# Optimization experiments

Measured on AMD Instinct MI355X. Metric: run time of the kernel, lower is better.

The kernel has to match this reference:

```python
import jax, jax.numpy as jnp
import numpy as np

D_MODEL = 1024
NUM_HEADS = 16
DEPTH = D_MODEL // NUM_HEADS


def setup_inputs() -> dict:
    key = jax.random.key(0)
    ks = jax.random.split(key, 9)
    B, S = 2, 2048
    s = 1.0 / np.sqrt(D_MODEL)
    return {
        "x": jax.random.normal(ks[0], (B, S, D_MODEL), dtype=jnp.float32),
        "wq": jax.random.normal(ks[1], (D_MODEL, D_MODEL), dtype=jnp.float32) * s,
        "bq": jnp.zeros((D_MODEL,), dtype=jnp.float32),
        "wk": jax.random.normal(ks[2], (D_MODEL, D_MODEL), dtype=jnp.float32) * s,
        "bk": jnp.zeros((D_MODEL,), dtype=jnp.float32),
        "wv": jax.random.normal(ks[3], (D_MODEL, D_MODEL), dtype=jnp.float32) * s,
        "bv": jnp.zeros((D_MODEL,), dtype=jnp.float32),
        "wo": jax.random.normal(ks[4], (D_MODEL, D_MODEL), dtype=jnp.float32) * s,
        "bo": jnp.zeros((D_MODEL,), dtype=jnp.float32),
    }


def _split_heads(t):
    # [B, S, D] -> [B, H, S, depth]
    B, S, _ = t.shape
    return t.reshape(B, S, NUM_HEADS, DEPTH).transpose(0, 2, 1, 3)


def reference(x, wq, bq, wk, bk, wv, bv, wo, bo):
    B, S, _ = x.shape
    q = _split_heads(x @ wq + bq)
    k = _split_heads(x @ wk + bk)
    v = _split_heads(x @ wv + bv)
    scale = 1.0 / jnp.sqrt(jnp.asarray(DEPTH, dtype=x.dtype))
    logits = jnp.einsum("bhsd,bhtd->bhst", q, k) * scale  # [B,H,S,S]
    attn = jax.nn.softmax(logits, axis=-1)
    ctx = jnp.einsum("bhst,bhtd->bhsd", attn, v)  # [B,H,S,depth]
    concat = ctx.transpose(0, 2, 1, 3).reshape(B, S, D_MODEL)
    return concat @ wo + bo
```

## Files before the change

### kernel.cpp

```cpp
#include <hip/hip_runtime.h>
#include <hip/hip_bf16.h>

typedef __bf16 bf16;
typedef __bf16 bf16x4 __attribute__((ext_vector_type(4)));
typedef __bf16 bf16x8 __attribute__((ext_vector_type(8)));
typedef float f32x4 __attribute__((ext_vector_type(4)));

typedef __attribute__((address_space(3))) void lds_void;
typedef const __attribute__((address_space(1))) void gbl_void;

#define D_MODEL 1024
#define NHEAD 16
#define DEPTH 64
#define SEQ 2048
#define BATCH 2
#define NTOK (BATCH * SEQ)

#define Q_SCALE 0.18033688f

__global__ __launch_bounds__(256) void prep(const float* __restrict__ w0,
                                            const float* __restrict__ w1,
                                            const float* __restrict__ w2,
                                            const float* __restrict__ w3,
                                            const float* __restrict__ x,
                                            bf16* __restrict__ wtb,
                                            bf16* __restrict__ xb) {
    int z = blockIdx.z;
    int tx = threadIdx.x, ty = threadIdx.y;
    if (z < 4) {
        const float* w = (z == 0) ? w0 : (z == 1) ? w1 : (z == 2) ? w2 : w3;
        bf16* d = wtb + (size_t)z * D_MODEL * D_MODEL;
        __shared__ float tile[32][33];
        int c0 = blockIdx.x * 32;
        int r0 = blockIdx.y * 32;
#pragma unroll
        for (int i = 0; i < 4; i++)
            tile[ty + i * 8][tx] = w[(size_t)(r0 + ty + i * 8) * D_MODEL + c0 + tx];
        __syncthreads();
#pragma unroll
        for (int i = 0; i < 4; i++)
            d[(size_t)(c0 + ty + i * 8) * D_MODEL + r0 + tx] = (bf16)tile[tx][ty + i * 8];
    } else {
        int t = ty * 32 + tx;
        size_t i = ((size_t)(z - 4) * 1024 + blockIdx.y * 32 + blockIdx.x) * 256 + t;
        float4 v = ((const float4*)x)[i];
        bf16x4 o = {(bf16)v.x, (bf16)v.y, (bf16)v.z, (bf16)v.w};
        *(bf16x4*)&xb[i * 4] = o;
    }
}

template <bool SWAP>
__device__ __forceinline__ void gemm_core128(const bf16* __restrict__ A,
                                             const bf16* __restrict__ Bt,
                                             int row0, int col0,
                                             bf16 (*sm)[2][8192],
                                             f32x4 acc[4][4]) {
    const int tid = threadIdx.x;
    const int lane = tid & 63;
    const int wave = tid >> 6;
    const int quad = lane >> 4, l16 = lane & 15;
    const int wm = (wave & 1) << 6, wn = (wave >> 1) << 6;
    const int sA = l16 & 7;
    const int scg = (tid & 7) ^ ((tid >> 3) & 7);

    const bf16* Ag = A + (size_t)(row0 + (tid >> 3)) * D_MODEL + scg * 8;
    const bf16* Bg = Bt + (size_t)(col0 + (tid >> 3)) * D_MODEL + scg * 8;

#define GLLQ(SRC, DST) __builtin_amdgcn_global_load_lds((gbl_void*)(SRC), (lds_void*)(DST), 16, 0, 0)
#define STGQ(BUF_, KB_) { \
    _Pragma("unroll") \
    for (int o_ = 0; o_ < 4; o_++) \
        GLLQ(Ag + (size_t)o_ * 32 * D_MODEL + (KB_), &sm[BUF_][0][o_ * 2048 + tid * 8]); \
    _Pragma("unroll") \
    for (int o_ = 0; o_ < 4; o_++) \
        GLLQ(Bg + (size_t)o_ * 32 * D_MODEL + (KB_), &sm[BUF_][1][o_ * 2048 + tid * 8]); }

    STGQ(0, 0);
#pragma unroll 1
    for (int t = 0; t < 16; t++) {
        if (t < 15) {
            STGQ((t + 1) & 1, (t + 1) * 64);
            asm volatile("s_waitcnt vmcnt(8)" ::: "memory");
        } else {
            asm volatile("s_waitcnt vmcnt(0)" ::: "memory");
        }
        __builtin_amdgcn_sched_barrier(0);
        __builtin_amdgcn_s_barrier();
        const int bs = t & 1;
#pragma unroll
        for (int kq = 0; kq < 2; kq++) {
            bf16x8 af[4], bfr[4];
            const int c = ((((kq << 2) | quad) ^ sA) << 3);
#pragma unroll
            for (int i = 0; i < 4; i++)
                af[i] = *(const bf16x8*)&sm[bs][0][(wm + i * 16 + l16) * 64 + c];
#pragma unroll
            for (int j = 0; j < 4; j++)
                bfr[j] = *(const bf16x8*)&sm[bs][1][(wn + j * 16 + l16) * 64 + c];
            __builtin_amdgcn_s_setprio(1);
#pragma unroll
            for (int i = 0; i < 4; i++)
#pragma unroll
                for (int j = 0; j < 4; j++)
                    acc[i][j] = SWAP
                        ? __builtin_amdgcn_mfma_f32_16x16x32_bf16(bfr[j], af[i], acc[i][j], 0, 0, 0)
                        : __builtin_amdgcn_mfma_f32_16x16x32_bf16(af[i], bfr[j], acc[i][j], 0, 0, 0);
            __builtin_amdgcn_s_setprio(0);
        }
        __builtin_amdgcn_sched_barrier(0);
        __builtin_amdgcn_s_barrier();
    }
#undef STGQ
#undef GLLQ
}

__global__ __launch_bounds__(256) void qkv_gemm(const bf16* __restrict__ xb,
                                                const bf16* __restrict__ wtb,
                                                const float* __restrict__ bq,
                                                const float* __restrict__ bk,
                                                const float* __restrict__ bv,
                                                bf16* __restrict__ q,
                                                bf16* __restrict__ k,
                                                bf16* __restrict__ v) {
    __shared__ __align__(16) bf16 sm[2][2][8192];
    int zc = blockIdx.x;
    int z = zc >> 3;
    const bf16* Bt = wtb + (size_t)z * D_MODEL * D_MODEL;
    const float* bias = (z == 0) ? bq : (z == 1) ? bk : bv;
    int row0 = blockIdx.y * 128, col0 = (zc & 7) * 128;
    f32x4 acc[4][4] = {};

    const int lane = threadIdx.x & 63, wave = threadIdx.x >> 6;
    const int quad = lane >> 4, l16 = lane & 15;
    const int wm = (wave & 1) << 6, wn = (wave >> 1) << 6;

    if (z < 2) {
        gemm_core128<false>(xb, Bt, row0, col0, sm, acc);
        bf16* dst = (z == 0) ? q : k;
        const float sc = (z == 0) ? Q_SCALE : 1.0f;
#pragma unroll
        for (int i = 0; i < 4; i++) {
#pragma unroll
            for (int j = 0; j < 4; j++) {
                int colg = col0 + wn + j * 16 + l16;
                int hh = colg >> 6, d = colg & 63;
                float bi = bias[colg];
                int rbase = row0 + wm + i * 16 + quad * 4;
                int b = rbase >> 11, sb = rbase & 2047;
#pragma unroll
                for (int r = 0; r < 4; r++) {
                    size_t idx = ((size_t)(b * NHEAD + hh) * SEQ + sb + r) * DEPTH + d;
                    dst[idx] = (bf16)((acc[i][j][r] + bi) * sc);
                }
            }
        }
    } else {
        gemm_core128<true>(xb, Bt, row0, col0, sm, acc);
#pragma unroll
        for (int i = 0; i < 4; i++) {
            int tok = row0 + wm + i * 16 + l16;
            int b = tok >> 11, sb = tok & 2047;
#pragma unroll
            for (int j = 0; j < 4; j++) {
#pragma unroll
                for (int r = 0; r < 4; r++) {
                    int f = col0 + wn + j * 16 + quad * 4 + r;
                    int hh = f >> 6, d = f & 63;
                    v[((size_t)(b * NHEAD + hh) * DEPTH + d) * SEQ + sb] =
                        (bf16)(acc[i][j][r] + bias[f]);
                }
            }
        }
    }
}

__global__ __launch_bounds__(512, 4) void attn(const bf16* __restrict__ q,
                                               const bf16* __restrict__ k,
                                               const bf16* __restrict__ v,
                                               bf16* __restrict__ ctx) {
    __shared__ __align__(16) bf16 smb[32768];
    const int tid = threadIdx.x;
    const int lane = tid & 63, wave = tid >> 6;
    const int ks = wave & 3, qg = wave >> 2;
    const int quad = lane >> 4, l16 = lane & 15;
    const int bh = blockIdx.x;
    const int q0 = blockIdx.y * 64;
    const size_t hb = (size_t)bh * SEQ * DEPTH;
    const bf16* qh = q + hb;
    const bf16* kh = k + hb;
    const bf16* vh = v + hb;

    bf16x8 bq_[2][2];
#pragma unroll
    for (int n = 0; n < 2; n++) {
        int qrow = q0 + qg * 32 + n * 16 + l16;
#pragma unroll
        for (int c = 0; c < 2; c++)
            bq_[n][c] = *(const bf16x8*)&qh[(size_t)qrow * DEPTH + c * 32 + quad * 8];
    }

    f32x4 ov[4][2] = {};
    float lvs[2] = {0.f, 0.f};

    const int sb = ks * 8192;
    const int kchS = (lane & 7) ^ (((lane >> 3) & 3) << 1);
    const int vchS = (lane & 3) ^ ((lane >> 3) & 3);
    const int krdL = ((l16 >> 2) << 3) + (l16 & 3);
    const int ksw = ((l16 & 3) << 1) | ((l16 >> 2) & 1);
    const int vsw = (quad ^ ((l16 >> 1) & 3)) << 3;

#define GLL(SRC, DST) __builtin_amdgcn_global_load_lds((gbl_void*)(SRC), (lds_void*)(DST), 16, 0, 0)

#define STAGE(BUF_, T_) { \
    _Pragma("unroll") \
    for (int o_ = 0; o_ < 4; o_++) { \
        const bf16* s_ = kh + (size_t)((T_) + ks * 32 + o_ * 8 + (lane >> 3)) * DEPTH \
                       + ((kchS ^ (o_ & 1)) << 3); \
        GLL(s_, smb + sb + (BUF_) * 2048 + o_ * 512 + lane * 8); \
    } \
    _Pragma("unroll") \
    for (int o_ = 0; o_ < 4; o_++) { \
        const bf16* s_ = vh + (size_t)(o_ * 16 + (lane >> 2)) * SEQ + (T_) + ks * 32 \
                       + (vchS << 3); \
        GLL(s_, smb + sb + 4096 + (BUF_) * 2048 + o_ * 512 + lane * 8); \
    } }

#define COMPUTE(BUF_) { \
    f32x4 s[2][2] = {}; \
    __builtin_amdgcn_s_setprio(1); \
    _Pragma("unroll") \
    for (int c_ = 0; c_ < 2; c_++) \
        _Pragma("unroll") \
        for (int h_ = 0; h_ < 2; h_++) { \
            bf16x8 kf = *(const bf16x8*)&smb[sb + (BUF_) * 2048 + (krdL + h_ * 4) * 64 \
                                             + ((((c_ << 2) | quad) ^ ksw) << 3)]; \
            _Pragma("unroll") \
            for (int n_ = 0; n_ < 2; n_++) \
                s[h_][n_] = __builtin_amdgcn_mfma_f32_16x16x32_bf16(kf, bq_[n_][c_], s[h_][n_], 0, 0, 0); \
        } \
    __builtin_amdgcn_s_setprio(0); \
    bf16x8 pb[2]; \
    _Pragma("unroll") \
    for (int n_ = 0; n_ < 2; n_++) { \
        float e0 = __builtin_amdgcn_exp2f(s[0][n_][0]); \
        float e1 = __builtin_amdgcn_exp2f(s[0][n_][1]); \
        float e2 = __builtin_amdgcn_exp2f(s[0][n_][2]); \
        float e3 = __builtin_amdgcn_exp2f(s[0][n_][3]); \
        float e4 = __builtin_amdgcn_exp2f(s[1][n_][0]); \
        float e5 = __builtin_amdgcn_exp2f(s[1][n_][1]); \
        float e6 = __builtin_amdgcn_exp2f(s[1][n_][2]); \
        float e7 = __builtin_amdgcn_exp2f(s[1][n_][3]); \
        pb[n_][0] = (bf16)e0; pb[n_][1] = (bf16)e1; \
        pb[n_][2] = (bf16)e2; pb[n_][3] = (bf16)e3; \
        pb[n_][4] = (bf16)e4; pb[n_][5] = (bf16)e5; \
        pb[n_][6] = (bf16)e6; pb[n_][7] = (bf16)e7; \
        lvs[n_] += ((e0 + e1) + (e2 + e3)) + ((e4 + e5) + (e6 + e7)); \
    } \
    __builtin_amdgcn_s_setprio(1); \
    _Pragma("unroll") \
    for (int t_ = 0; t_ < 4; t_++) { \
        bf16x8 vf = *(const bf16x8*)&smb[sb + 4096 + (BUF_) * 2048 + (t_ * 16 + l16) * 32 + vsw]; \
        _Pragma("unroll") \
        for (int n_ = 0; n_ < 2; n_++) \
            ov[t_][n_] = __builtin_amdgcn_mfma_f32_16x16x32_bf16(vf, pb[n_], ov[t_][n_], 0, 0, 0); \
    } \
    __builtin_amdgcn_s_setprio(0); }

#define SB0 __builtin_amdgcn_sched_barrier(0)

    if (qg == 0) STAGE(0, 0);
#pragma unroll 1
    for (int i = 0; i < 16; i++) {
        if (qg == 0) {
            if (i < 15) {
                STAGE((i + 1) & 1, (i + 1) * 128);
                asm volatile("s_waitcnt vmcnt(8)" ::: "memory");
            } else {
                asm volatile("s_waitcnt vmcnt(0)" ::: "memory");
            }
        }
        SB0;
        __builtin_amdgcn_s_barrier();
        COMPUTE(i & 1);
        SB0;
        __builtin_amdgcn_s_barrier();
    }

#undef SB0
#undef COMPUTE
#undef STAGE
#undef GLL

    f32x4* Red  = (f32x4*)smb;
    float* Lred = (float*)((char*)smb + 32768);
    const int b = bh >> 4, hh = bh & 15;
    const int tA = ks >> 1, nA = ks & 1;

    __syncthreads();
#pragma unroll
    for (int t2 = 0; t2 < 2; t2++)
#pragma unroll
        for (int n = 0; n < 2; n++)
            Red[((((qg * 2 + t2) * 2 + n) * 4) + ks) * 64 + lane] = ov[t2][n];
#pragma unroll
    for (int n = 0; n < 2; n++)
        Lred[((qg * 2 + n) * 4 + ks) * 64 + lane] = lvs[n];
    __syncthreads();

    float ls0 = 0.f, ls1 = 0.f;
#pragma unroll
    for (int k4 = 0; k4 < 4; k4++)
#pragma unroll
        for (int qd = 0; qd < 4; qd++) {
            ls0 += Lred[((qg * 2 + 0) * 4 + k4) * 64 + qd * 16 + l16];
            ls1 += Lred[((qg * 2 + 1) * 4 + k4) * 64 + qd * 16 + l16];
        }
    const float lsn = (ks & 1) ? ls1 : ls0;
    const float iv = 1.0f / lsn;

    {
        f32x4 sv = Red[((((qg * 2 + tA) * 2 + nA) * 4) + 0) * 64 + lane]
                 + Red[((((qg * 2 + tA) * 2 + nA) * 4) + 1) * 64 + lane]
                 + Red[((((qg * 2 + tA) * 2 + nA) * 4) + 2) * 64 + lane]
                 + Red[((((qg * 2 + tA) * 2 + nA) * 4) + 3) * 64 + lane];
        bf16x4 ob = {(bf16)(sv[0] * iv), (bf16)(sv[1] * iv),
                     (bf16)(sv[2] * iv), (bf16)(sv[3] * iv)};
        size_t off = ((size_t)(b * SEQ + q0 + qg * 32 + nA * 16 + l16)) * D_MODEL
                   + hh * 64 + tA * 16 + quad * 4;
        *(bf16x4*)&ctx[off] = ob;
    }
    __syncthreads();
#pragma unroll
    for (int t2 = 0; t2 < 2; t2++)
#pragma unroll
        for (int n = 0; n < 2; n++)
            Red[((((qg * 2 + t2) * 2 + n) * 4) + ks) * 64 + lane] = ov[2 + t2][n];
    __syncthreads();
    {
        f32x4 sv = Red[((((qg * 2 + tA) * 2 + nA) * 4) + 0) * 64 + lane]
                 + Red[((((qg * 2 + tA) * 2 + nA) * 4) + 1) * 64 + lane]
                 + Red[((((qg * 2 + tA) * 2 + nA) * 4) + 2) * 64 + lane]
                 + Red[((((qg * 2 + tA) * 2 + nA) * 4) + 3) * 64 + lane];
        bf16x4 ob = {(bf16)(sv[0] * iv), (bf16)(sv[1] * iv),
                     (bf16)(sv[2] * iv), (bf16)(sv[3] * iv)};
        size_t off = ((size_t)(b * SEQ + q0 + qg * 32 + nA * 16 + l16)) * D_MODEL
                   + hh * 64 + (2 + tA) * 16 + quad * 4;
        *(bf16x4*)&ctx[off] = ob;
    }
}

__global__ __launch_bounds__(256) void out_gemm(const bf16* __restrict__ ctx,
                                                const bf16* __restrict__ wot,
                                                const float* __restrict__ bo,
                                                float* __restrict__ out) {
    __shared__ bf16 As[64 * 32];
    __shared__ bf16 Bs[128 * 32];
    const int tid = threadIdx.x;
    const int lane = tid & 63, wave = tid >> 6;
    const int quad = lane >> 4, l16 = lane & 15;
    const int srow = lane >> 2, selem = (lane & 3) * 8;
    int row0 = blockIdx.y * 64, col0 = blockIdx.x * 128;
    f32x4 acc[4][2] = {};

    for (int k0 = 0; k0 < D_MODEL; k0 += 32) {
        __syncthreads();
        {
            const bf16* ga = ctx + (size_t)(row0 + wave * 16 + srow) * D_MODEL + k0 + selem;
            __builtin_amdgcn_global_load_lds((gbl_void*)ga, (lds_void*)(As + wave * 512 + lane * 8), 16, 0, 0);
        }
#pragma unroll
        for (int t = 0; t < 2; t++) {
            int m = wave * 2 + t;
            const bf16* gb = wot + (size_t)(col0 + m * 16 + srow) * D_MODEL + k0 + selem;
            __builtin_amdgcn_global_load_lds((gbl_void*)gb, (lds_void*)(Bs + m * 512 + lane * 8), 16, 0, 0);
        }
        __syncthreads();
        bf16x8 af[4], bfr[2];
#pragma unroll
        for (int i = 0; i < 4; i++)
            af[i] = *(const bf16x8*)&As[(i * 16 + l16) * 32 + quad * 8];
#pragma unroll
        for (int j = 0; j < 2; j++)
            bfr[j] = *(const bf16x8*)&Bs[(wave * 32 + j * 16 + l16) * 32 + quad * 8];
#pragma unroll
        for (int i = 0; i < 4; i++)
#pragma unroll
            for (int j = 0; j < 2; j++)
                acc[i][j] = __builtin_amdgcn_mfma_f32_16x16x32_bf16(af[i], bfr[j], acc[i][j], 0, 0, 0);
    }
#pragma unroll
    for (int i = 0; i < 4; i++)
#pragma unroll
        for (int j = 0; j < 2; j++) {
            int colg = col0 + wave * 32 + j * 16 + l16;
            float bi = bo[colg];
            int rbase = row0 + i * 16 + quad * 4;
#pragma unroll
            for (int r = 0; r < 4; r++)
                out[(size_t)(rbase + r) * D_MODEL + colg] = acc[i][j][r] + bi;
        }
}

extern "C" void kernel_launch(void* const* d_in, const int* in_sizes, int n_in,
                              void* d_out, int out_size, void* d_ws, size_t ws_size,
                              hipStream_t stream) {
    const float* x  = (const float*)d_in[0];
    const float* wq = (const float*)d_in[1];
    const float* bq = (const float*)d_in[2];
    const float* wk = (const float*)d_in[3];
    const float* bk = (const float*)d_in[4];
    const float* wv = (const float*)d_in[5];
    const float* bv = (const float*)d_in[6];
    const float* wo = (const float*)d_in[7];
    const float* bo = (const float*)d_in[8];
    float* out = (float*)d_out;

    const size_t MB = 1024 * 1024;
    char* ws = (char*)d_ws;
    bf16* xb  = (bf16*)(ws);
    bf16* wtb = (bf16*)(ws + 8 * MB);
    bf16* qb  = (bf16*)(ws + 16 * MB);
    bf16* kb  = (bf16*)(ws + 24 * MB);
    bf16* vb  = (bf16*)(ws + 32 * MB);
    bf16* ctx = (bf16*)(ws + 40 * MB);

    prep<<<dim3(32, 32, 8), dim3(32, 8), 0, stream>>>(wq, wk, wv, wo, x, wtb, xb);
    qkv_gemm<<<dim3(24, 32), 256, 0, stream>>>(xb, wtb, bq, bk, bv, qb, kb, vb);
    attn<<<dim3(BATCH * NHEAD, SEQ / 64), dim3(512), 0, stream>>>(qb, kb, vb, ctx);
    out_gemm<<<dim3(8, 64), 256, 0, stream>>>(ctx, wtb + 3 * (size_t)D_MODEL * D_MODEL, bo, out);
}
```

Before: 184.6 us.

## Double-buffer LDS tiles in output projection GEMM to overlap loads with MFMA

The output projection GEMM now keeps two LDS buffers for its A and B tiles and issues the global-to-LDS loads for the next K step before computing the current one. It uses explicit vmcnt waits and raw s_barrier calls in place of two __syncthreads per iteration, and raises wave priority around the MFMA block. The goal is to hide global load latency behind matrix math in this one kernel, at the cost of doubled LDS use and hand-managed synchronisation that could be fragile.

```diff
diff --git a/kernel.cpp b/kernel.cpp
--- a/kernel.cpp
+++ b/kernel.cpp
@@ -353,8 +353,8 @@
                                                 const bf16* __restrict__ wot,
                                                 const float* __restrict__ bo,
                                                 float* __restrict__ out) {
-    __shared__ bf16 As[64 * 32];
-    __shared__ bf16 Bs[128 * 32];
+    __shared__ __align__(16) bf16 As[2][64 * 32];
+    __shared__ __align__(16) bf16 Bs[2][128 * 32];
     const int tid = threadIdx.x;
     const int lane = tid & 63, wave = tid >> 6;
     const int quad = lane >> 4, l16 = lane & 15;
@@ -362,32 +362,48 @@
     int row0 = blockIdx.y * 64, col0 = blockIdx.x * 128;
     f32x4 acc[4][2] = {};
 
-    for (int k0 = 0; k0 < D_MODEL; k0 += 32) {
-        __syncthreads();
-        {
-            const bf16* ga = ctx + (size_t)(row0 + wave * 16 + srow) * D_MODEL + k0 + selem;
-            __builtin_amdgcn_global_load_lds((gbl_void*)ga, (lds_void*)(As + wave * 512 + lane * 8), 16, 0, 0);
-        }
-#pragma unroll
-        for (int t = 0; t < 2; t++) {
-            int m = wave * 2 + t;
-            const bf16* gb = wot + (size_t)(col0 + m * 16 + srow) * D_MODEL + k0 + selem;
-            __builtin_amdgcn_global_load_lds((gbl_void*)gb, (lds_void*)(Bs + m * 512 + lane * 8), 16, 0, 0);
-        }
-        __syncthreads();
+    const bf16* Ag = ctx + (size_t)(row0 + wave * 16 + srow) * D_MODEL + selem;
+    const bf16* Bg0 = wot + (size_t)(col0 + (wave * 2 + 0) * 16 + srow) * D_MODEL + selem;
+    const bf16* Bg1 = wot + (size_t)(col0 + (wave * 2 + 1) * 16 + srow) * D_MODEL + selem;
+
+#define GLLO(SRC, DST) __builtin_amdgcn_global_load_lds((gbl_void*)(SRC), (lds_void*)(DST), 16, 0, 0)
+#define STGO(BUF_, K_) { \
+    GLLO(Ag + (K_), (lds_void*)(&As[BUF_][0] + wave * 512 + lane * 8)); \
+    GLLO(Bg0 + (K_), (lds_void*)(&Bs[BUF_][0] + (wave * 2 + 0) * 512 + lane * 8)); \
+    GLLO(Bg1 + (K_), (lds_void*)(&Bs[BUF_][0] + (wave * 2 + 1) * 512 + lane * 8)); }
+
+    STGO(0, 0);
+#pragma unroll 1
+    for (int kk = 0; kk < 32; kk++) {
+        if (kk < 31) {
+            STGO((kk + 1) & 1, (kk + 1) * 32);
+            asm volatile("s_waitcnt vmcnt(3)" ::: "memory");
+        } else {
+            asm volatile("s_waitcnt vmcnt(0)" ::: "memory");
+        }
+        __builtin_amdgcn_sched_barrier(0);
+        __builtin_amdgcn_s_barrier();
+        const int bs = kk & 1;
         bf16x8 af[4], bfr[2];
 #pragma unroll
         for (int i = 0; i < 4; i++)
-            af[i] = *(const bf16x8*)&As[(i * 16 + l16) * 32 + quad * 8];
+            af[i] = *(const bf16x8*)&As[bs][(i * 16 + l16) * 32 + quad * 8];
 #pragma unroll
         for (int j = 0; j < 2; j++)
-            bfr[j] = *(const bf16x8*)&Bs[(wave * 32 + j * 16 + l16) * 32 + quad * 8];
+            bfr[j] = *(const bf16x8*)&Bs[bs][(wave * 32 + j * 16 + l16) * 32 + quad * 8];
+        __builtin_amdgcn_s_setprio(1);
 #pragma unroll
         for (int i = 0; i < 4; i++)
 #pragma unroll
             for (int j = 0; j < 2; j++)
                 acc[i][j] = __builtin_amdgcn_mfma_f32_16x16x32_bf16(af[i], bfr[j], acc[i][j], 0, 0, 0);
-    }
+        __builtin_amdgcn_s_setprio(0);
+        __builtin_amdgcn_sched_barrier(0);
+        __builtin_amdgcn_s_barrier();
+    }
+#undef STGO
+#undef GLLO
+
 #pragma unroll
     for (int i = 0; i < 4; i++)
 #pragma unroll
```

Result: no change. 187.4 us (+1.5%).
